# Kernel optimization log

Measured on AMD Instinct MI355X. Metric: run time of the kernel, lower is better.

The kernel has to match this reference:

```python
import jax, jax.numpy as jnp
import numpy as np

IN_FEATURES = 128
OUT_FEATURES = 32
N_NODES = 2048
ALPHA = 0.2  # LeakyReLU negative slope
NEG_INF = -9e15


def setup_inputs() -> dict:
    key = jax.random.key(0)
    k1, k2, k3, k4 = jax.random.split(key, 4)
    h = jax.random.normal(k1, (N_NODES, IN_FEATURES), dtype=jnp.float32)
    adj = jax.random.randint(k2, (N_NODES, N_NODES), 0, 2, dtype=jnp.int32)
    # xavier_uniform-ish scaling for params
    W = jax.random.normal(k3, (2 * IN_FEATURES, OUT_FEATURES), dtype=jnp.float32) * 0.1
    a = jax.random.normal(k4, (OUT_FEATURES,), dtype=jnp.float32) * 0.2
    return {"h": h, "adj": adj, "W": W, "a": a}


def reference(h, adj, W, a):
    in_f = h.shape[1]
    Wh1 = h @ W[:in_f, :]   # [N, F]
    Wh2 = h @ W[in_f:, :]   # [N, F]
    # GATv2 score: e[i,k] = sum_f a[f] * leaky_relu(Wh1[i,f] + Wh2[k,f])
    e = jax.nn.leaky_relu(Wh1[:, None, :] + Wh2[None, :, :], negative_slope=ALPHA)  # [N, N, F]
    e = jnp.einsum('ikf,f->ik', e, a)  # [N, N]
    att = jnp.where(adj > 0, e, NEG_INF)
    att = jax.nn.softmax(att, axis=1)
    h_prime = att @ Wh1  # note: original aggregates Wh1, faithful to source
    return jax.nn.elu(h_prime)  # concat=True -> ELU
```

## Files before the change

kernel.cpp:

```cpp
#include <hip/hip_runtime.h>
#include <math.h>

#define N_NODES 2048
#define IN_F 128
#define OUT_F 32
#define ALPHA 0.2f
#define NEG_INF -9e15f
#define TI 4

__global__ __launch_bounds__(256) void precompute_wh(
    const float* __restrict__ h, const float* __restrict__ W,
    float* __restrict__ Wh1, float* __restrict__ Wh2)
{
    __shared__ float h_s[8][IN_F];
    const int t = threadIdx.x;
    const int i0 = blockIdx.x * 8;

    #pragma unroll
    for (int j = 0; j < 4; ++j) {
        int e = t + 256 * j;
        h_s[e >> 7][e & 127] = h[i0 * IN_F + e];
    }
    __syncthreads();

    const int f = t & 31;
    const int r = t >> 5;
    float acc1 = 0.f, acc2 = 0.f;
    #pragma unroll 4
    for (int c = 0; c < IN_F; ++c) {
        float hv = h_s[r][c];
        acc1 += hv * W[c * OUT_F + f];
        acc2 += hv * W[(IN_F + c) * OUT_F + f];
    }
    Wh1[(i0 + r) * OUT_F + f] = acc1;
    Wh2[(i0 + r) * OUT_F + f] = acc2;
}

__global__ __launch_bounds__(256) void gat_row(
    const float* __restrict__ Wh1, const float* __restrict__ Wh2,
    const int* __restrict__ adj, const float* __restrict__ a,
    float* __restrict__ out)
{
    __shared__ float s_s[TI][N_NODES];
    __shared__ float w1s[TI][OUT_F];
    __shared__ float a_s[OUT_F];
    __shared__ float wred[TI][4];
    __shared__ float Ms[TI], Ls[TI];
    __shared__ float part[8][TI][OUT_F];

    const int t = threadIdx.x;
    const int i0 = blockIdx.x * TI;

    if (t < TI * OUT_F) w1s[t >> 5][t & 31] = Wh1[i0 * OUT_F + t];
    if (t < OUT_F) a_s[t] = a[t];
    __syncthreads();

    float areg[OUT_F];
    #pragma unroll
    for (int f = 0; f < OUT_F; ++f) areg[f] = a_s[f];

    float m0 = NEG_INF, m1 = NEG_INF, m2 = NEG_INF, m3 = NEG_INF;
    for (int kc = 0; kc < 8; ++kc) {
        const int k = t + 256 * kc;
        const float4* w2v = (const float4*)(Wh2 + k * OUT_F);
        float acc0 = 0.f, acc1 = 0.f, acc2 = 0.f, acc3 = 0.f;
        #pragma unroll
        for (int j = 0; j < 8; ++j) {
            float4 q = w2v[j];
            #pragma unroll
            for (int e = 0; e < 4; ++e) {
                const int f = 4 * j + e;
                const float wf = (e == 0) ? q.x : (e == 1) ? q.y : (e == 2) ? q.z : q.w;
                const float af = areg[f];
                float x;
                x = w1s[0][f] + wf; acc0 += af * fmaxf(x, ALPHA * x);
                x = w1s[1][f] + wf; acc1 += af * fmaxf(x, ALPHA * x);
                x = w1s[2][f] + wf; acc2 += af * fmaxf(x, ALPHA * x);
                x = w1s[3][f] + wf; acc3 += af * fmaxf(x, ALPHA * x);
            }
        }
        const int base = i0 * N_NODES + k;
        float s0 = (adj[base + 0 * N_NODES] > 0) ? acc0 : NEG_INF;
        float s1 = (adj[base + 1 * N_NODES] > 0) ? acc1 : NEG_INF;
        float s2 = (adj[base + 2 * N_NODES] > 0) ? acc2 : NEG_INF;
        float s3 = (adj[base + 3 * N_NODES] > 0) ? acc3 : NEG_INF;
        s_s[0][k] = s0; m0 = fmaxf(m0, s0);
        s_s[1][k] = s1; m1 = fmaxf(m1, s1);
        s_s[2][k] = s2; m2 = fmaxf(m2, s2);
        s_s[3][k] = s3; m3 = fmaxf(m3, s3);
    }

    const int lane = t & 63, wid = t >> 6;
    #pragma unroll
    for (int off = 32; off > 0; off >>= 1) {
        m0 = fmaxf(m0, __shfl_down(m0, off, 64));
        m1 = fmaxf(m1, __shfl_down(m1, off, 64));
        m2 = fmaxf(m2, __shfl_down(m2, off, 64));
        m3 = fmaxf(m3, __shfl_down(m3, off, 64));
    }
    if (lane == 0) { wred[0][wid] = m0; wred[1][wid] = m1; wred[2][wid] = m2; wred[3][wid] = m3; }
    __syncthreads();
    if (t < TI) {
        Ms[t] = fmaxf(fmaxf(wred[t][0], wred[t][1]), fmaxf(wred[t][2], wred[t][3]));
    }
    __syncthreads();

    const float M0 = Ms[0], M1 = Ms[1], M2 = Ms[2], M3 = Ms[3];
    float l0 = 0.f, l1 = 0.f, l2 = 0.f, l3 = 0.f;
    for (int kc = 0; kc < 8; ++kc) {
        const int k = t + 256 * kc;
        float p0 = __expf(s_s[0][k] - M0); s_s[0][k] = p0; l0 += p0;
        float p1 = __expf(s_s[1][k] - M1); s_s[1][k] = p1; l1 += p1;
        float p2 = __expf(s_s[2][k] - M2); s_s[2][k] = p2; l2 += p2;
        float p3 = __expf(s_s[3][k] - M3); s_s[3][k] = p3; l3 += p3;
    }
    #pragma unroll
    for (int off = 32; off > 0; off >>= 1) {
        l0 += __shfl_down(l0, off, 64);
        l1 += __shfl_down(l1, off, 64);
        l2 += __shfl_down(l2, off, 64);
        l3 += __shfl_down(l3, off, 64);
    }
    __syncthreads();
    if (lane == 0) { wred[0][wid] = l0; wred[1][wid] = l1; wred[2][wid] = l2; wred[3][wid] = l3; }
    __syncthreads();
    if (t < TI) {
        Ls[t] = wred[t][0] + wred[t][1] + wred[t][2] + wred[t][3];
    }
    __syncthreads();

    const int f = t & 31, c = t >> 5;
    float acc0 = 0.f, acc1 = 0.f, acc2 = 0.f, acc3 = 0.f;
    const int k0 = c * 256;
    #pragma unroll 4
    for (int kk = 0; kk < 256; ++kk) {
        const int k = k0 + kk;
        const float wv = Wh1[k * OUT_F + f];
        acc0 += s_s[0][k] * wv;
        acc1 += s_s[1][k] * wv;
        acc2 += s_s[2][k] * wv;
        acc3 += s_s[3][k] * wv;
    }
    part[c][0][f] = acc0;
    part[c][1][f] = acc1;
    part[c][2][f] = acc2;
    part[c][3][f] = acc3;
    __syncthreads();

    if (t < TI * OUT_F) {
        const int ii = t >> 5, ff = t & 31;
        float sum = 0.f;
        #pragma unroll
        for (int c2 = 0; c2 < 8; ++c2) sum += part[c2][ii][ff];
        const float val = sum / Ls[ii];
        out[(i0 + ii) * OUT_F + ff] = (val > 0.f) ? val : (__expf(val) - 1.f);
    }
}

extern "C" void kernel_launch(void* const* d_in, const int* in_sizes, int n_in,
                              void* d_out, int out_size, void* d_ws, size_t ws_size,
                              hipStream_t stream) {
    const float* h   = (const float*)d_in[0];
    const int*   adj = (const int*)d_in[1];
    const float* W   = (const float*)d_in[2];
    const float* a   = (const float*)d_in[3];
    float* out = (float*)d_out;

    float* Wh1 = (float*)d_ws;
    float* Wh2 = Wh1 + N_NODES * OUT_F;

    precompute_wh<<<N_NODES / 8, 256, 0, stream>>>(h, W, Wh1, Wh2);
    gat_row<<<N_NODES / TI, 256, 0, stream>>>(Wh1, Wh2, adj, a, out);
}
```

Before: 122.0 us.

## Rewrite LeakyReLU score via abs identity, shrink row tile to two rows

Rewrites leaky_relu(x) as 0.6x+0.4|x|. The linear part becomes a per-neighbour term Q[k] plus a per-row constant that cancels in the softmax, so the inner loop is one add, one abs and one FMA per feature. Q and the scaled weight vector C are computed in the precompute kernel. The attention kernel now handles 2 rows per block (1024 blocks) and each thread processes two neighbours. Scores stay in registers instead of shared memory, the probabilities go to an XOR-swizzled shared buffer, and adj/Q are read as vector loads with xor-shuffle reductions. The aggregation is re-tiled into 16 chunks, each thread producing two output features for both rows. The trade-offs are slight floating-point differences from the reassociation and reading C from global memory inside the hot loop.

```diff
diff --git a/kernel.cpp b/kernel.cpp
--- a/kernel.cpp
+++ b/kernel.cpp
@@ -4,155 +4,170 @@
 #define N_NODES 2048
 #define IN_F 128
 #define OUT_F 32
-#define ALPHA 0.2f
 #define NEG_INF -9e15f
-#define TI 4
+
+__device__ __forceinline__ int swz(int k) { return k ^ (((k >> 7) & 7) << 2); }
 
 __global__ __launch_bounds__(256) void precompute_wh(
     const float* __restrict__ h, const float* __restrict__ W,
-    float* __restrict__ Wh1, float* __restrict__ Wh2)
+    const float* __restrict__ a,
+    float* __restrict__ Wh1, float* __restrict__ Wh2,
+    float* __restrict__ Q, float* __restrict__ C)
 {
     __shared__ float h_s[8][IN_F];
     const int t = threadIdx.x;
     const int i0 = blockIdx.x * 8;
 
-    #pragma unroll
-    for (int j = 0; j < 4; ++j) {
-        int e = t + 256 * j;
-        h_s[e >> 7][e & 127] = h[i0 * IN_F + e];
-    }
+    ((float4*)&h_s[0][0])[t] = ((const float4*)(h + (size_t)i0 * IN_F))[t];
     __syncthreads();
 
     const int f = t & 31;
     const int r = t >> 5;
     float acc1 = 0.f, acc2 = 0.f;
-    #pragma unroll 4
+    #pragma unroll 8
     for (int c = 0; c < IN_F; ++c) {
-        float hv = h_s[r][c];
-        acc1 += hv * W[c * OUT_F + f];
-        acc2 += hv * W[(IN_F + c) * OUT_F + f];
+        const float hv = h_s[r][c];
+        acc1 = fmaf(hv, W[c * OUT_F + f], acc1);
+        acc2 = fmaf(hv, W[(IN_F + c) * OUT_F + f], acc2);
     }
     Wh1[(i0 + r) * OUT_F + f] = acc1;
     Wh2[(i0 + r) * OUT_F + f] = acc2;
+
+    float q = 0.6f * a[f] * acc2;
+    #pragma unroll
+    for (int off = 16; off > 0; off >>= 1) q += __shfl_xor(q, off, 64);
+    if (f == 0) Q[i0 + r] = q;
+
+    if (blockIdx.x == 0 && t < OUT_F) C[t] = 0.4f * a[t];
 }
 
-__global__ __launch_bounds__(256) void gat_row(
+__global__ __launch_bounds__(256, 4) void gat_row(
     const float* __restrict__ Wh1, const float* __restrict__ Wh2,
-    const int* __restrict__ adj, const float* __restrict__ a,
-    float* __restrict__ out)
+    const float* __restrict__ Q, const float* __restrict__ C,
+    const int* __restrict__ adj, float* __restrict__ out)
 {
-    __shared__ float s_s[TI][N_NODES];
-    __shared__ float w1s[TI][OUT_F];
-    __shared__ float a_s[OUT_F];
-    __shared__ float wred[TI][4];
-    __shared__ float Ms[TI], Ls[TI];
-    __shared__ float part[8][TI][OUT_F];
+    __shared__ float p_s[2 * N_NODES];
+    __shared__ float w1s[2][OUT_F];
+    __shared__ float part[16][2][OUT_F];
+    __shared__ float redA[4], redB[4], redC[4], redD[4];
 
     const int t = threadIdx.x;
-    const int i0 = blockIdx.x * TI;
+    const int i0 = blockIdx.x * 2;
 
-    if (t < TI * OUT_F) w1s[t >> 5][t & 31] = Wh1[i0 * OUT_F + t];
-    if (t < OUT_F) a_s[t] = a[t];
+    if (t < 2 * OUT_F) w1s[t >> 5][t & 31] = Wh1[i0 * OUT_F + t];
     __syncthreads();
 
-    float areg[OUT_F];
+    const float4* w1f0 = (const float4*)&w1s[0][0];
+    const float4* w1f1 = (const float4*)&w1s[1][0];
+
+    float s00[4], s01[4], s10[4], s11[4];
+    float m0 = NEG_INF, m1 = NEG_INF;
+
     #pragma unroll
-    for (int f = 0; f < OUT_F; ++f) areg[f] = a_s[f];
-
-    float m0 = NEG_INF, m1 = NEG_INF, m2 = NEG_INF, m3 = NEG_INF;
-    for (int kc = 0; kc < 8; ++kc) {
-        const int k = t + 256 * kc;
-        const float4* w2v = (const float4*)(Wh2 + k * OUT_F);
-        float acc0 = 0.f, acc1 = 0.f, acc2 = 0.f, acc3 = 0.f;
+    for (int kc = 0; kc < 4; ++kc) {
+        const int k = 2 * t + 512 * kc;
+        const float4* wr = (const float4*)(Wh2 + (size_t)k * OUT_F);
+        float a00 = 0.f, a01 = 0.f, a10 = 0.f, a11 = 0.f;
         #pragma unroll
         for (int j = 0; j < 8; ++j) {
-            float4 q = w2v[j];
+            const float4 w1a = w1f0[j];
+            const float4 w1b = w1f1[j];
+            const float4 qa = wr[j];
+            const float4 qb = wr[8 + j];
             #pragma unroll
             for (int e = 0; e < 4; ++e) {
-                const int f = 4 * j + e;
-                const float wf = (e == 0) ? q.x : (e == 1) ? q.y : (e == 2) ? q.z : q.w;
-                const float af = areg[f];
-                float x;
-                x = w1s[0][f] + wf; acc0 += af * fmaxf(x, ALPHA * x);
-                x = w1s[1][f] + wf; acc1 += af * fmaxf(x, ALPHA * x);
-                x = w1s[2][f] + wf; acc2 += af * fmaxf(x, ALPHA * x);
-                x = w1s[3][f] + wf; acc3 += af * fmaxf(x, ALPHA * x);
+                const float cf  = C[4 * j + e];
+                const float w2a = (e==0)?qa.x:(e==1)?qa.y:(e==2)?qa.z:qa.w;
+                const float w2b = (e==0)?qb.x:(e==1)?qb.y:(e==2)?qb.z:qb.w;
+                const float w10 = (e==0)?w1a.x:(e==1)?w1a.y:(e==2)?w1a.z:w1a.w;
+                const float w11 = (e==0)?w1b.x:(e==1)?w1b.y:(e==2)?w1b.z:w1b.w;
+                a00 = fmaf(cf, fabsf(w10 + w2a), a00);
+                a01 = fmaf(cf, fabsf(w10 + w2b), a01);
+                a10 = fmaf(cf, fabsf(w11 + w2a), a10);
+                a11 = fmaf(cf, fabsf(w11 + w2b), a11);
             }
         }
-        const int base = i0 * N_NODES + k;
-        float s0 = (adj[base + 0 * N_NODES] > 0) ? acc0 : NEG_INF;
-        float s1 = (adj[base + 1 * N_NODES] > 0) ? acc1 : NEG_INF;
-        float s2 = (adj[base + 2 * N_NODES] > 0) ? acc2 : NEG_INF;
-        float s3 = (adj[base + 3 * N_NODES] > 0) ? acc3 : NEG_INF;
-        s_s[0][k] = s0; m0 = fmaxf(m0, s0);
-        s_s[1][k] = s1; m1 = fmaxf(m1, s1);
-        s_s[2][k] = s2; m2 = fmaxf(m2, s2);
-        s_s[3][k] = s3; m3 = fmaxf(m3, s3);
+        const int2 ad0   = *(const int2*)(adj + (size_t)(i0 + 0) * N_NODES + k);
+        const int2 ad1   = *(const int2*)(adj + (size_t)(i0 + 1) * N_NODES + k);
+        const float2 qk  = *(const float2*)(Q + k);
+        const float v00 = (ad0.x > 0) ? a00 + qk.x : NEG_INF;
+        const float v01 = (ad0.y > 0) ? a01 + qk.y : NEG_INF;
+        const float v10 = (ad1.x > 0) ? a10 + qk.x : NEG_INF;
+        const float v11 = (ad1.y > 0) ? a11 + qk.y : NEG_INF;
+        s00[kc] = v00; s01[kc] = v01; s10[kc] = v10; s11[kc] = v11;
+        m0 = fmaxf(m0, fmaxf(v00, v01));
+        m1 = fmaxf(m1, fmaxf(v10, v11));
     }
 
-    const int lane = t & 63, wid = t >> 6;
     #pragma unroll
     for (int off = 32; off > 0; off >>= 1) {
-        m0 = fmaxf(m0, __shfl_down(m0, off, 64));
-        m1 = fmaxf(m1, __shfl_down(m1, off, 64));
-        m2 = fmaxf(m2, __shfl_down(m2, off, 64));
-        m3 = fmaxf(m3, __shfl_down(m3, off, 64));
+        m0 = fmaxf(m0, __shfl_xor(m0, off, 64));
+        m1 = fmaxf(m1, __shfl_xor(m1, off, 64));
     }
-    if (lane == 0) { wred[0][wid] = m0; wred[1][wid] = m1; wred[2][wid] = m2; wred[3][wid] = m3; }
+    const int lane = t & 63, wid = t >> 6;
+    if (lane == 0) { redA[wid] = m0; redB[wid] = m1; }
     __syncthreads();
-    if (t < TI) {
-        Ms[t] = fmaxf(fmaxf(wred[t][0], wred[t][1]), fmaxf(wred[t][2], wred[t][3]));
-    }
-    __syncthreads();
+    const float M0 = fmaxf(fmaxf(redA[0], redA[1]), fmaxf(redA[2], redA[3]));
+    const float M1 = fmaxf(fmaxf(redB[0], redB[1]), fmaxf(redB[2], redB[3]));
 
-    const float M0 = Ms[0], M1 = Ms[1], M2 = Ms[2], M3 = Ms[3];
-    float l0 = 0.f, l1 = 0.f, l2 = 0.f, l3 = 0.f;
-    for (int kc = 0; kc < 8; ++kc) {
-        const int k = t + 256 * kc;
-        float p0 = __expf(s_s[0][k] - M0); s_s[0][k] = p0; l0 += p0;
-        float p1 = __expf(s_s[1][k] - M1); s_s[1][k] = p1; l1 += p1;
-        float p2 = __expf(s_s[2][k] - M2); s_s[2][k] = p2; l2 += p2;
-        float p3 = __expf(s_s[3][k] - M3); s_s[3][k] = p3; l3 += p3;
+    float l0 = 0.f, l1 = 0.f;
+    #pragma unroll
+    for (int kc = 0; kc < 4; ++kc) {
+        const int k = 2 * t + 512 * kc;
+        const float p00 = __expf(s00[kc] - M0);
+        const float p01 = __expf(s01[kc] - M0);
+        const float p10 = __expf(s10[kc] - M1);
+        const float p11 = __expf(s11[kc] - M1);
+        *(float2*)&p_s[swz(k)]           = make_float2(p00, p01);
+        *(float2*)&p_s[N_NODES + swz(k)] = make_float2(p10, p11);
+        l0 += p00 + p01;
+        l1 += p10 + p11;
     }
     #pragma unroll
     for (int off = 32; off > 0; off >>= 1) {
-        l0 += __shfl_down(l0, off, 64);
-        l1 += __shfl_down(l1, off, 64);
-        l2 += __shfl_down(l2, off, 64);
-        l3 += __shfl_down(l3, off, 64);
+        l0 += __shfl_xor(l0, off, 64);
+        l1 += __shfl_xor(l1, off, 64);
     }
+    if (lane == 0) { redC[wid] = l0; redD[wid] = l1; }
     __syncthreads();
-    if (lane == 0) { wred[0][wid] = l0; wred[1][wid] = l1; wred[2][wid] = l2; wred[3][wid] = l3; }
-    __syncthreads();
-    if (t < TI) {
-        Ls[t] = wred[t][0] + wred[t][1] + wred[t][2] + wred[t][3];
+    const float L0 = redC[0] + redC[1] + redC[2] + redC[3];
+    const float L1 = redD[0] + redD[1] + redD[2] + redD[3];
+
+    const int f2 = t & 15;
+    const int c  = t >> 4;
+    float acc00 = 0.f, acc01 = 0.f, acc10 = 0.f, acc11 = 0.f;
+    const int kb = c * 128;
+    #pragma unroll 4
+    for (int it = 0; it < 32; ++it) {
+        const int k = kb + 4 * it;
+        const float4 p0 = *(const float4*)&p_s[swz(k)];
+        const float4 p1 = *(const float4*)&p_s[N_NODES + swz(k)];
+        const float* wrow = Wh1 + (size_t)k * OUT_F + f2;
+        const float wa0 = wrow[0],  wb0 = wrow[16];
+        const float wa1 = wrow[32], wb1 = wrow[48];
+        const float wa2 = wrow[64], wb2 = wrow[80];
+        const float wa3 = wrow[96], wb3 = wrow[112];
+        acc00 = fmaf(p0.x, wa0, acc00); acc01 = fmaf(p0.x, wb0, acc01);
+        acc10 = fmaf(p1.x, wa0, acc10); acc11 = fmaf(p1.x, wb0, acc11);
+        acc00 = fmaf(p0.y, wa1, acc00); acc01 = fmaf(p0.y, wb1, acc01);
+        acc10 = fmaf(p1.y, wa1, acc10); acc11 = fmaf(p1.y, wb1, acc11);
+        acc00 = fmaf(p0.z, wa2, acc00); acc01 = fmaf(p0.z, wb2, acc01);
+        acc10 = fmaf(p1.z, wa2, acc10); acc11 = fmaf(p1.z, wb2, acc11);
+        acc00 = fmaf(p0.w, wa3, acc00); acc01 = fmaf(p0.w, wb3, acc01);
+        acc10 = fmaf(p1.w, wa3, acc10); acc11 = fmaf(p1.w, wb3, acc11);
     }
+    part[c][0][f2]      = acc00;
+    part[c][0][f2 + 16] = acc01;
+    part[c][1][f2]      = acc10;
+    part[c][1][f2 + 16] = acc11;
     __syncthreads();
 
-    const int f = t & 31, c = t >> 5;
-    float acc0 = 0.f, acc1 = 0.f, acc2 = 0.f, acc3 = 0.f;
-    const int k0 = c * 256;
-    #pragma unroll 4
-    for (int kk = 0; kk < 256; ++kk) {
-        const int k = k0 + kk;
-        const float wv = Wh1[k * OUT_F + f];
-        acc0 += s_s[0][k] * wv;
-        acc1 += s_s[1][k] * wv;
-        acc2 += s_s[2][k] * wv;
-        acc3 += s_s[3][k] * wv;
-    }
-    part[c][0][f] = acc0;
-    part[c][1][f] = acc1;
-    part[c][2][f] = acc2;
-    part[c][3][f] = acc3;
-    __syncthreads();
-
-    if (t < TI * OUT_F) {
+    if (t < 2 * OUT_F) {
         const int ii = t >> 5, ff = t & 31;
-        float sum = 0.f;
+        float s = 0.f;
         #pragma unroll
-        for (int c2 = 0; c2 < 8; ++c2) sum += part[c2][ii][ff];
-        const float val = sum / Ls[ii];
+        for (int c2 = 0; c2 < 16; ++c2) s += part[c2][ii][ff];
+        const float val = s / (ii == 0 ? L0 : L1);
         out[(i0 + ii) * OUT_F + ff] = (val > 0.f) ? val : (__expf(val) - 1.f);
     }
 }
@@ -168,7 +183,9 @@
 
     float* Wh1 = (float*)d_ws;
     float* Wh2 = Wh1 + N_NODES * OUT_F;
+    float* Q   = Wh2 + N_NODES * OUT_F;
+    float* C   = Q + N_NODES;
 
-    precompute_wh<<<N_NODES / 8, 256, 0, stream>>>(h, W, Wh1, Wh2);
-    gat_row<<<N_NODES / TI, 256, 0, stream>>>(Wh1, Wh2, adj, a, out);
+    precompute_wh<<<N_NODES / 8, 256, 0, stream>>>(h, W, a, Wh1, Wh2, Q, C);
+    gat_row<<<N_NODES / 2, 256, 0, stream>>>(Wh1, Wh2, Q, C, adj, out);
 }
```

New measurement: 125.2 us. 1.03x slower.
